# Kernel optimization log

Hardware: AMD Instinct MI355X
Metric: run time of the kernel (lower is better)

## Reference

```python
import jax, jax.numpy as jnp
import numpy as np

FS = 16000.0
SOUND_SPEED = 343.0
MAX_ORDER = 10
FILTER_LEN = 81            # fractional-delay sinc filter taps (torchaudio default)
PAD = FILTER_LEN // 2      # 40
RIR_LEN = 8000             # static RIR length; bounds max delay for 10 m rooms, order 10

# ---- static image-source lattice: all (i,j,k) with |i|+|j|+|k| <= MAX_ORDER ----
_ind = np.arange(-MAX_ORDER, MAX_ORDER + 1)
_g = np.stack(np.meshgrid(_ind, _ind, _ind, indexing="ij"), -1).reshape(-1, 3)
_g = _g[np.abs(_g).sum(-1) <= MAX_ORDER]                      # (n_img=1561, 3)
XYZ = jnp.asarray(_g, dtype=jnp.float32)                      # (n_img, 3)
EXP_LO = jnp.asarray(np.abs(np.floor(_g / 2.0)), jnp.float32)        # reflections off x=0/y=0/z=0 walls
EXP_HI = jnp.asarray(np.abs(np.floor((_g + 1) / 2.0)), jnp.float32)  # reflections off far walls
ODD = jnp.asarray(_g % 2 == 1)                                # (n_img, 3) bool


def _hann(x, T):
    # truncated Hann window used by the fractional-delay filter
    return jnp.where(jnp.abs(x) <= T / 2, 0.5 * (1.0 + jnp.cos(2.0 * jnp.pi * x / T)), 0.0)


def _rir_one(room, mic, src, absorption):
    # room, mic, src: (3,) metres; absorption: (6,) per-wall absorption coeff
    # image-source positions: mirror source across walls per parity of lattice index
    img = jnp.where(ODD, room * (XYZ + 1.0) - src, room * XYZ + src)   # (n_img, 3)
    tr = jnp.sqrt(1.0 - absorption)                                     # wall reflection coeffs (6,)
    att = jnp.prod((tr[::2] ** EXP_LO) * (tr[1::2] ** EXP_HI), axis=-1)  # (n_img,)
    dist = jnp.linalg.norm(img - mic, axis=-1)                           # (n_img,)
    amp = att / dist                                                     # 1/r spreading
    delay = dist * FS / SOUND_SPEED                                      # delay in samples (float)
    delay_i = jnp.ceil(delay)                                            # integer anchor
    n = jnp.arange(-PAD, PAD + 1, dtype=jnp.float32)                     # (81,)
    x = n[None, :] + delay_i[:, None] - delay[:, None]                   # (n_img, 81)
    irs = amp[:, None] * jnp.sinc(x) * _hann(x, 2 * PAD)                 # windowed-sinc frac delay
    # scatter-add each 81-tap filter at offset delay_i - PAD into the RIR buffer
    idx = delay_i.astype(jnp.int32)[:, None] - PAD + jnp.arange(FILTER_LEN, dtype=jnp.int32)
    valid = (idx >= 0) & (idx < RIR_LEN)
    rir = jnp.zeros((RIR_LEN,), irs.dtype).at[jnp.clip(idx, 0, RIR_LEN - 1)].add(
        jnp.where(valid, irs, 0.0))
    return rir


def setup_inputs() -> dict:
    key = jax.random.key(0)
    k1, k2, k3, k4 = jax.random.split(key, 4)
    B = 256
    room = 3.0 + 7.0 * jax.random.uniform(k1, (B, 3), jnp.float32)       # room dims in [3,10] m
    mic_f = 0.05 + 0.40 * jax.random.uniform(k2, (B, 3), jnp.float32)    # mic frac in [0.05,0.45]
    src_f = 0.55 + 0.40 * jax.random.uniform(k3, (B, 3), jnp.float32)    # src frac in [0.55,0.95]
    absorp = 0.1 + 0.4 * jax.random.uniform(k4, (B, 1), jnp.float32)     # absorption in [0.1,0.5]
    inp = jnp.concatenate([room, mic_f, src_f, absorp], axis=1)          # (B, 10)
    return {"input": inp}


def reference(input):
    room = input[:, 0:3]
    mic = input[:, 3:6] * room
    src = input[:, 6:9] * room
    absorption = jnp.repeat(input[:, 9:10], 6, axis=1)                   # uniform over 6 walls
    rir = jax.vmap(_rir_one)(room, mic, src, absorption)                 # (B, RIR_LEN)
    dist = jnp.linalg.norm(mic - src, axis=1)
    toa = 40.0 + FS * dist / SOUND_SPEED                                 # (B,)
    return rir, toa
```

## Files before the change

kernel.cpp:

```cpp
#include <hip/hip_runtime.h>
#include <math.h>

#define NB 256
#define NIMG 1561
#define RIRLEN 8000
#define FLEN 81
#define PADI 40
#define NTHREADS 1024
#define NSEG 125
#define NBUCKET 126

struct ImgTab { unsigned int v[NIMG]; };

constexpr ImgTab build_tab() {
    ImgTab t{};
    int n = 0;
    for (int x = -10; x <= 10; ++x)
        for (int y = -10; y <= 10; ++y)
            for (int z = -10; z <= 10; ++z) {
                int ax = x < 0 ? -x : x;
                int ay = y < 0 ? -y : y;
                int az = z < 0 ? -z : z;
                int l1 = ax + ay + az;
                if (l1 <= 10) {
                    t.v[n++] = (unsigned)(x + 10) | ((unsigned)(y + 10) << 5) |
                               ((unsigned)(z + 10) << 10) | ((unsigned)l1 << 15);
                }
            }
    return t;
}

constexpr int tab_count() {
    int n = 0;
    for (int x = -10; x <= 10; ++x)
        for (int y = -10; y <= 10; ++y)
            for (int z = -10; z <= 10; ++z) {
                int ax = x < 0 ? -x : x;
                int ay = y < 0 ? -y : y;
                int az = z < 0 ? -z : z;
                if (ax + ay + az <= 10) ++n;
            }
    return n;
}
static_assert(tab_count() == NIMG, "image count mismatch");

__constant__ ImgTab c_tab = build_tab();

__global__ __launch_bounds__(NTHREADS) void
rir_kernel(const float* __restrict__ in, float* __restrict__ out) {
    __shared__ float4 s_rec[NIMG];
    __shared__ float  s_trpow[11];
    __shared__ int    s_hist[NBUCKET];
    __shared__ int    s_start[NBUCKET + 1];
    __shared__ int    s_cursor[NBUCKET];
    __shared__ int    s_scan[128];

    const int b   = blockIdx.x;
    const int tid = threadIdx.x;
    const float* p = in + b * 10;

    if (tid < NBUCKET) s_hist[tid] = 0;
    if (tid == 0) {
        float tr = sqrtf(1.0f - p[9]);
        float pw = 1.0f;
        for (int k = 0; k <= 10; ++k) { s_trpow[k] = pw; pw *= tr; }
    }
    __syncthreads();

    const float rx = p[0], ry = p[1], rz = p[2];
    const float mx = p[3] * rx, my = p[4] * ry, mz = p[5] * rz;
    const float sx = p[6] * rx, sy = p[7] * ry, sz = p[8] * rz;
    const float K = 16000.0f / 343.0f;
    const float INV_PI = 0.31830988618379067154f;

    float4 rec[2];
    int ibase[2] = {0, 0};
    int ibkt[2]  = {0, 0};
    bool ivalid[2] = {false, false};

    for (int u = 0; u < 2; ++u) {
        int i = tid + u * NTHREADS;
        if (i < NIMG) {
            unsigned v = c_tab.v[i];
            int gx = (int)(v & 31u) - 10;
            int gy = (int)((v >> 5) & 31u) - 10;
            int gz = (int)((v >> 10) & 31u) - 10;
            int l1 = (int)(v >> 15);

            float ix = (gx & 1) ? rx * (float)(gx + 1) - sx : rx * (float)gx + sx;
            float iy = (gy & 1) ? ry * (float)(gy + 1) - sy : ry * (float)gy + sy;
            float iz = (gz & 1) ? rz * (float)(gz + 1) - sz : rz * (float)gz + sz;

            float dx = ix - mx, dy = iy - my, dz = iz - mz;
            float dist = sqrtf(dx * dx + dy * dy + dz * dz);

            float amp  = s_trpow[l1] / dist;
            float d    = dist * K;
            float dlc  = ceilf(d);
            float frac = dlc - d;
            int   idlc = (int)dlc;
            int   base = idlc - PADI;

            if (base < RIRLEN) {
                float frb = fmaxf(frac, 9.5367431640625e-7f);
                float spf = (frb < 1.0e-3f) ? frb : (sinpif(frb) * INV_PI);
                float S   = amp * spf;
                if (idlc & 1) S = -S;
                float db  = dlc - frb;
                rec[u] = make_float4(S,
                                     cospif(db * 0.025f),
                                     sinpif(db * 0.025f),
                                     db);
                ibase[u]  = base;
                ibkt[u]   = (base + 64) >> 6;
                ivalid[u] = true;
                atomicAdd(&s_hist[ibkt[u]], 1);
            }
        }
    }
    __syncthreads();

    if (tid < 128) s_scan[tid] = (tid < NBUCKET) ? s_hist[tid] : 0;
    __syncthreads();
    for (int d = 1; d < 128; d <<= 1) {
        int y = 0;
        if (tid < 128 && tid >= d) y = s_scan[tid - d];
        __syncthreads();
        if (tid < 128) s_scan[tid] += y;
        __syncthreads();
    }
    if (tid < NBUCKET) {
        s_start[tid + 1] = s_scan[tid];
        s_cursor[tid]    = (tid == 0) ? 0 : s_scan[tid - 1];
        if (tid == 0) s_start[0] = 0;
    }
    __syncthreads();

    for (int u = 0; u < 2; ++u) {
        if (ivalid[u]) {
            int pos = atomicAdd(&s_cursor[ibkt[u]], 1);
            s_rec[pos] = rec[u];
        }
    }
    __syncthreads();

    const int wave = tid >> 6;
    const int lane = tid & 63;
    for (int s = wave; s < NSEG; s += NTHREADS / 64) {
        const int   n_i = (s << 6) + lane;
        const float fn  = (float)n_i;
        const float cn = cospif(fn * 0.025f);
        const float sn = sinpif(fn * 0.025f);
        float acc = 0.0f;

        int b0 = (s > 0) ? (s - 1) : 0;
        int b1 = (s + 1 < NBUCKET) ? (s + 1) : (NBUCKET - 1);
        int lo = s_start[b0], hi = s_start[b1 + 1];
#pragma clang loop unroll_count(4)
        for (int k = lo; k < hi; ++k) {
            float4 r = s_rec[k];
            float x  = fn - r.w;
            float ax = fabsf(x);
            float xb = (x == 0.0f) ? 9.5367431640625e-7f : x;
            float hc = fmaf(cn, r.y, sn * r.z);
            float hann = fmaf(0.5f, hc, 0.5f);
            hann = (ax < 40.0f) ? hann : 0.0f;
            acc  = fmaf(r.x * __builtin_amdgcn_rcpf(xb), hann, acc);
        }
        float sgn = (n_i & 1) ? -1.0f : 1.0f;
        out[(size_t)b * RIRLEN + n_i] = acc * sgn;
    }

    if (tid == 0) {
        float dx = mx - sx, dy = my - sy, dz = mz - sz;
        out[(size_t)NB * RIRLEN + b] = 40.0f + sqrtf(dx * dx + dy * dy + dz * dz) * K;
    }
}

extern "C" void kernel_launch(void* const* d_in, const int* in_sizes, int n_in,
                              void* d_out, int out_size, void* d_ws, size_t ws_size,
                              hipStream_t stream) {
    const float* in = (const float*)d_in[0];
    float* out = (float*)d_out;
    rir_kernel<<<dim3(NB), dim3(NTHREADS), 0, stream>>>(in, out);
}
```

Measured before the change: 86.22 us.

## Split RIR into prep and gather kernels with finer 16-sample buckets

Splits the single fused kernel into two. A prep kernel computes the image records and bucket offsets and writes them to workspace memory. A gather kernel, launched with four blocks per batch, evaluates output samples from global memory. Buckets shrink from 64 to 16 samples, so each 64-sample segment scans fewer records outside the filter window. The cost is a second launch, a round trip through global memory instead of LDS, and a longer scan in the prep kernel.

```diff
diff --git a/kernel.cpp b/kernel.cpp
--- a/kernel.cpp
+++ b/kernel.cpp
@@ -4,11 +4,9 @@
 #define NB 256
 #define NIMG 1561
 #define RIRLEN 8000
-#define FLEN 81
 #define PADI 40
-#define NTHREADS 1024
-#define NSEG 125
-#define NBUCKET 126
+#define NBKT 505
+#define NSTART (NBKT + 1)
 
 struct ImgTab { unsigned int v[NIMG]; };
 
@@ -46,20 +44,21 @@
 
 __constant__ ImgTab c_tab = build_tab();
 
-__global__ __launch_bounds__(NTHREADS) void
-rir_kernel(const float* __restrict__ in, float* __restrict__ out) {
-    __shared__ float4 s_rec[NIMG];
-    __shared__ float  s_trpow[11];
-    __shared__ int    s_hist[NBUCKET];
-    __shared__ int    s_start[NBUCKET + 1];
-    __shared__ int    s_cursor[NBUCKET];
-    __shared__ int    s_scan[128];
+
+__global__ __launch_bounds__(1024) void
+prep_kernel(const float* __restrict__ in, float4* __restrict__ g_rec,
+            int* __restrict__ g_start, float* __restrict__ out) {
+    __shared__ float s_trpow[11];
+    __shared__ int   s_hist[NBKT];
+    __shared__ int   s_scan[512];
+    __shared__ int   s_start[NSTART];
+    __shared__ int   s_cursor[NBKT];
 
     const int b   = blockIdx.x;
     const int tid = threadIdx.x;
     const float* p = in + b * 10;
 
-    if (tid < NBUCKET) s_hist[tid] = 0;
+    if (tid < NBKT) s_hist[tid] = 0;
     if (tid == 0) {
         float tr = sqrtf(1.0f - p[9]);
         float pw = 1.0f;
@@ -74,12 +73,11 @@
     const float INV_PI = 0.31830988618379067154f;
 
     float4 rec[2];
-    int ibase[2] = {0, 0};
     int ibkt[2]  = {0, 0};
     bool ivalid[2] = {false, false};
 
     for (int u = 0; u < 2; ++u) {
-        int i = tid + u * NTHREADS;
+        int i = tid + u * 1024;
         if (i < NIMG) {
             unsigned v = c_tab.v[i];
             int gx = (int)(v & 31u) - 10;
@@ -107,12 +105,8 @@
                 float S   = amp * spf;
                 if (idlc & 1) S = -S;
                 float db  = dlc - frb;
-                rec[u] = make_float4(S,
-                                     cospif(db * 0.025f),
-                                     sinpif(db * 0.025f),
-                                     db);
-                ibase[u]  = base;
-                ibkt[u]   = (base + 64) >> 6;
+                rec[u] = make_float4(S, cospif(db * 0.025f), sinpif(db * 0.025f), db);
+                ibkt[u]   = (base + 80) >> 4;
                 ivalid[u] = true;
                 atomicAdd(&s_hist[ibkt[u]], 1);
             }
@@ -120,45 +114,63 @@
     }
     __syncthreads();
 
-    if (tid < 128) s_scan[tid] = (tid < NBUCKET) ? s_hist[tid] : 0;
+    if (tid < 512) s_scan[tid] = (tid < NBKT) ? s_hist[tid] : 0;
     __syncthreads();
-    for (int d = 1; d < 128; d <<= 1) {
+    for (int d = 1; d < 512; d <<= 1) {
         int y = 0;
-        if (tid < 128 && tid >= d) y = s_scan[tid - d];
+        if (tid < 512 && tid >= d) y = s_scan[tid - d];
         __syncthreads();
-        if (tid < 128) s_scan[tid] += y;
+        if (tid < 512) s_scan[tid] += y;
         __syncthreads();
     }
-    if (tid < NBUCKET) {
+    if (tid < NBKT) {
         s_start[tid + 1] = s_scan[tid];
         s_cursor[tid]    = (tid == 0) ? 0 : s_scan[tid - 1];
         if (tid == 0) s_start[0] = 0;
     }
     __syncthreads();
 
+    if (tid < NSTART) g_start[b * NSTART + tid] = s_start[tid];
+
+    float4* recb = g_rec + (size_t)b * NIMG;
     for (int u = 0; u < 2; ++u) {
         if (ivalid[u]) {
             int pos = atomicAdd(&s_cursor[ibkt[u]], 1);
-            s_rec[pos] = rec[u];
+            recb[pos] = rec[u];
         }
     }
-    __syncthreads();
 
-    const int wave = tid >> 6;
-    const int lane = tid & 63;
-    for (int s = wave; s < NSEG; s += NTHREADS / 64) {
+    if (tid == 0) {
+        float dx = mx - sx, dy = my - sy, dz = mz - sz;
+        out[(size_t)NB * RIRLEN + b] = 40.0f + sqrtf(dx * dx + dy * dy + dz * dz) * K;
+    }
+}
+
+__global__ __launch_bounds__(256) void
+gather_kernel(const float4* __restrict__ g_rec, const int* __restrict__ g_start,
+              float* __restrict__ out) {
+    const int b    = blockIdx.x >> 2;
+    const int part = blockIdx.x & 3;
+    const int wave = threadIdx.x >> 6;
+    const int lane = threadIdx.x & 63;
+
+    const float4* __restrict__ rec = g_rec + (size_t)b * NIMG;
+    const int*    __restrict__ st  = g_start + b * NSTART;
+    float* __restrict__ ob = out + (size_t)b * RIRLEN;
+
+    const int s_end = (part * 32 + 32 < 125) ? part * 32 + 32 : 125;
+    for (int s = part * 32 + wave; s < s_end; s += 4) {
         const int   n_i = (s << 6) + lane;
         const float fn  = (float)n_i;
-        const float cn = cospif(fn * 0.025f);
-        const float sn = sinpif(fn * 0.025f);
+        const float cn  = cospif(fn * 0.025f);
+        const float sn  = sinpif(fn * 0.025f);
         float acc = 0.0f;
 
-        int b0 = (s > 0) ? (s - 1) : 0;
-        int b1 = (s + 1 < NBUCKET) ? (s + 1) : (NBUCKET - 1);
-        int lo = s_start[b0], hi = s_start[b1 + 1];
+        int lo = __builtin_amdgcn_readfirstlane(st[4 * s]);
+        int hi = __builtin_amdgcn_readfirstlane(st[4 * s + 9]);
 #pragma clang loop unroll_count(4)
         for (int k = lo; k < hi; ++k) {
-            float4 r = s_rec[k];
+            float4 r = rec[k];
             float x  = fn - r.w;
             float ax = fabsf(x);
             float xb = (x == 0.0f) ? 9.5367431640625e-7f : x;
@@ -168,12 +180,7 @@
             acc  = fmaf(r.x * __builtin_amdgcn_rcpf(xb), hann, acc);
         }
         float sgn = (n_i & 1) ? -1.0f : 1.0f;
-        out[(size_t)b * RIRLEN + n_i] = acc * sgn;
-    }
-
-    if (tid == 0) {
-        float dx = mx - sx, dy = my - sy, dz = mz - sz;
-        out[(size_t)NB * RIRLEN + b] = 40.0f + sqrtf(dx * dx + dy * dy + dz * dz) * K;
+        ob[n_i] = acc * sgn;
     }
 }
 
@@ -182,5 +189,9 @@
                               hipStream_t stream) {
     const float* in = (const float*)d_in[0];
     float* out = (float*)d_out;
-    rir_kernel<<<dim3(NB), dim3(NTHREADS), 0, stream>>>(in, out);
+    float4* g_rec = (float4*)d_ws;
+    int* g_start = (int*)((char*)d_ws + (size_t)NB * NIMG * sizeof(float4));
+
+    prep_kernel<<<dim3(NB), dim3(1024), 0, stream>>>(in, g_rec, g_start, out);
+    gather_kernel<<<dim3(NB * 4), dim3(256), 0, stream>>>(g_rec, g_start, out);
 }
```

After: 148.7 us. 72.4% more time.

## Use finer 16-sample buckets, two outputs per lane, and separate integer-delay spikes

Applied to the files above, without the earlier changes.

Image-source records are sorted into 16-sample buckets instead of 64, so each output segment scans a tighter candidate list. Each lane now computes two outputs per loaded record, and the half-waves share a trip count padded with a zero sentinel record. Hann and amplitude factors are folded into the record so the inner loop has fewer operations. Images with exactly integer delay are handled as spikes added atomically afterwards, which adds a barrier and global atomics and caps spikes at 64.

```diff
diff --git a/kernel.cpp b/kernel.cpp
--- a/kernel.cpp
+++ b/kernel.cpp
@@ -4,11 +4,11 @@
 #define NB 256
 #define NIMG 1561
 #define RIRLEN 8000
-#define FLEN 81
 #define PADI 40
 #define NTHREADS 1024
-#define NSEG 125
-#define NBUCKET 126
+#define NBKT 505
+#define NSTARTP 512
+#define NPAIR 63
 
 struct ImgTab { unsigned int v[NIMG]; };
 
@@ -48,22 +48,27 @@
 
 __global__ __launch_bounds__(NTHREADS) void
 rir_kernel(const float* __restrict__ in, float* __restrict__ out) {
-    __shared__ float4 s_rec[NIMG];
+    __shared__ float4 s_rec[NIMG + 1];
     __shared__ float  s_trpow[11];
-    __shared__ int    s_hist[NBUCKET];
-    __shared__ int    s_start[NBUCKET + 1];
-    __shared__ int    s_cursor[NBUCKET];
-    __shared__ int    s_scan[128];
+    __shared__ int    s_hist[NBKT];
+    __shared__ int    s_scan[512];
+    __shared__ int    s_start[NSTARTP];
+    __shared__ int    s_cursor[NBKT];
+    __shared__ int    s_nspike;
+    __shared__ int    s_spike_idx[64];
+    __shared__ float  s_spike_amp[64];
 
     const int b   = blockIdx.x;
     const int tid = threadIdx.x;
     const float* p = in + b * 10;
 
-    if (tid < NBUCKET) s_hist[tid] = 0;
+    if (tid < NBKT) s_hist[tid] = 0;
     if (tid == 0) {
         float tr = sqrtf(1.0f - p[9]);
         float pw = 1.0f;
         for (int k = 0; k <= 10; ++k) { s_trpow[k] = pw; pw *= tr; }
+        s_nspike = 0;
+        s_rec[NIMG] = make_float4(0.0f, 0.0f, 0.0f, -1.0e6f);
     }
     __syncthreads();
 
@@ -74,7 +79,6 @@
     const float INV_PI = 0.31830988618379067154f;
 
     float4 rec[2];
-    int ibase[2] = {0, 0};
     int ibkt[2]  = {0, 0};
     bool ivalid[2] = {false, false};
 
@@ -102,38 +106,43 @@
             int   base = idlc - PADI;
 
             if (base < RIRLEN) {
-                float frb = fmaxf(frac, 9.5367431640625e-7f);
-                float spf = (frb < 1.0e-3f) ? frb : (sinpif(frb) * INV_PI);
-                float S   = amp * spf;
-                if (idlc & 1) S = -S;
-                float db  = dlc - frb;
-                rec[u] = make_float4(S,
-                                     cospif(db * 0.025f),
-                                     sinpif(db * 0.025f),
-                                     db);
-                ibase[u]  = base;
-                ibkt[u]   = (base + 64) >> 6;
-                ivalid[u] = true;
-                atomicAdd(&s_hist[ibkt[u]], 1);
+                if (frac == 0.0f) {
+                    if (idlc < RIRLEN) {
+                        int sp = atomicAdd(&s_nspike, 1);
+                        if (sp < 64) { s_spike_idx[sp] = idlc; s_spike_amp[sp] = amp; }
+                    }
+                } else {
+                    float spf = (frac < 1.0e-3f) ? frac : (sinpif(frac) * INV_PI);
+                    float S   = amp * spf;
+                    if (idlc & 1) S = -S;
+                    float hS  = 0.5f * S;
+                    float cd  = cospif(d * 0.025f);
+                    float sd  = sinpif(d * 0.025f);
+                    rec[u] = make_float4(hS, hS * cd, hS * sd, d);
+                    ibkt[u]   = (base + 80) >> 4;
+                    ivalid[u] = true;
+                    atomicAdd(&s_hist[ibkt[u]], 1);
+                }
             }
         }
     }
     __syncthreads();
 
-    if (tid < 128) s_scan[tid] = (tid < NBUCKET) ? s_hist[tid] : 0;
-    __syncthreads();
-    for (int d = 1; d < 128; d <<= 1) {
+    if (tid < 512) s_scan[tid] = (tid < NBKT) ? s_hist[tid] : 0;
+    __syncthreads();
+    for (int d = 1; d < 512; d <<= 1) {
         int y = 0;
-        if (tid < 128 && tid >= d) y = s_scan[tid - d];
+        if (tid < 512 && tid >= d) y = s_scan[tid - d];
         __syncthreads();
-        if (tid < 128) s_scan[tid] += y;
+        if (tid < 512) s_scan[tid] += y;
         __syncthreads();
     }
-    if (tid < NBUCKET) {
+    if (tid < NBKT) {
         s_start[tid + 1] = s_scan[tid];
         s_cursor[tid]    = (tid == 0) ? 0 : s_scan[tid - 1];
         if (tid == 0) s_start[0] = 0;
     }
+    if (tid >= NBKT + 1 && tid < NSTARTP) s_start[tid] = s_scan[NBKT - 1];
     __syncthreads();
 
     for (int u = 0; u < 2; ++u) {
@@ -146,30 +155,47 @@
 
     const int wave = tid >> 6;
     const int lane = tid & 63;
-    for (int s = wave; s < NSEG; s += NTHREADS / 64) {
-        const int   n_i = (s << 6) + lane;
-        const float fn  = (float)n_i;
-        const float cn = cospif(fn * 0.025f);
-        const float sn = sinpif(fn * 0.025f);
-        float acc = 0.0f;
-
-        int b0 = (s > 0) ? (s - 1) : 0;
-        int b1 = (s + 1 < NBUCKET) ? (s + 1) : (NBUCKET - 1);
-        int lo = s_start[b0], hi = s_start[b1 + 1];
+    const int h    = lane >> 5;
+    const int l5   = lane & 31;
+    float* __restrict__ ob = out + (size_t)b * RIRLEN;
+
+    for (int q = wave; q < NPAIR; q += NTHREADS / 64) {
+        const int s  = 2 * q + h;
+        const int n0 = (q << 7) + (h << 6) + l5;
+        const int n1 = n0 + 32;
+        const float fn0 = (float)n0, fn1 = (float)n1;
+        const float cn0 = cospif(fn0 * 0.025f), sn0 = sinpif(fn0 * 0.025f);
+        const float cn1 = cospif(fn1 * 0.025f), sn1 = sinpif(fn1 * 0.025f);
+
+        const int lo = s_start[4 * s];
+        const int hi = s_start[4 * s + 9];
+        int lenA = __shfl(hi - lo, 0);
+        int lenB = __shfl(hi - lo, 32);
+        const int trips = (lenA > lenB) ? lenA : lenB;
+
+        float acc0 = 0.0f, acc1 = 0.0f;
+        int k = lo;
 #pragma clang loop unroll_count(4)
-        for (int k = lo; k < hi; ++k) {
-            float4 r = s_rec[k];
-            float x  = fn - r.w;
-            float ax = fabsf(x);
-            float xb = (x == 0.0f) ? 9.5367431640625e-7f : x;
-            float hc = fmaf(cn, r.y, sn * r.z);
-            float hann = fmaf(0.5f, hc, 0.5f);
-            hann = (ax < 40.0f) ? hann : 0.0f;
-            acc  = fmaf(r.x * __builtin_amdgcn_rcpf(xb), hann, acc);
+        for (int it = 0; it < trips; ++it, ++k) {
+            int kc = (k < hi) ? k : NIMG;
+            float4 r = s_rec[kc];
+            float x0 = fn0 - r.w;
+            float x1 = fn1 - r.w;
+            float t0 = fmaf(r.y, cn0, r.x); t0 = fmaf(r.z, sn0, t0);
+            float t1 = fmaf(r.y, cn1, r.x); t1 = fmaf(r.z, sn1, t1);
+            t0 = (fabsf(x0) < 40.0f) ? t0 : 0.0f;
+            t1 = (fabsf(x1) < 40.0f) ? t1 : 0.0f;
+            acc0 = fmaf(t0, __builtin_amdgcn_rcpf(x0), acc0);
+            acc1 = fmaf(t1, __builtin_amdgcn_rcpf(x1), acc1);
         }
-        float sgn = (n_i & 1) ? -1.0f : 1.0f;
-        out[(size_t)b * RIRLEN + n_i] = acc * sgn;
-    }
+        const float sgn = (n0 & 1) ? -1.0f : 1.0f;
+        if (n0 < RIRLEN) ob[n0] = acc0 * sgn;
+        if (n1 < RIRLEN) ob[n1] = acc1 * sgn;
+    }
+
+    __syncthreads();
+    int nsp = s_nspike; nsp = (nsp < 64) ? nsp : 64;
+    if (tid < nsp) atomicAdd(&ob[s_spike_idx[tid]], s_spike_amp[tid]);
 
     if (tid == 0) {
         float dx = mx - sx, dy = my - sy, dz = mz - sz;
```

After: 83.49 us. 3.2% less time.
